# Kernel tuning notes

Measured on AMD Instinct MI355X. Metric: run time of the kernel, lower is better.

The kernel has to match this reference:

```python
import jax, jax.numpy as jnp
import numpy as np

A = -0.75  # cv2 INTER_CUBIC cubic-convolution coefficient

def _cubic_kernel(d):
    d = jnp.abs(d)
    return jnp.where(
        d <= 1.0, (A + 2.0) * d**3 - (A + 3.0) * d**2 + 1.0,
        jnp.where(d < 2.0, A * d**3 - 5.0 * A * d**2 + 8.0 * A * d - 4.0 * A, 0.0))

def _resize_last_axis(x, s):
    # Bicubic upsample along the last axis by integer factor s (half-pixel
    # aligned, replicate border), matching cv2.resize INTER_CUBIC semantics.
    n = x.shape[-1]
    out_n = n * s
    src = (jnp.arange(out_n, dtype=jnp.float32) + 0.5) / s - 0.5
    base = jnp.floor(src).astype(jnp.int32)
    t = src - base.astype(jnp.float32)
    offs = jnp.arange(-1, 3)                      # 4 taps
    w = _cubic_kernel(t[:, None] - offs[None, :].astype(jnp.float32))  # [out_n,4]
    idx = jnp.clip(base[:, None] + offs[None, :], 0, n - 1)            # [out_n,4]
    g = x[..., idx]                                # [..., out_n, 4]
    return jnp.einsum('...ok,ok->...o', g, w)

def bicubic_upscale(x, s):
    # x: [B,C,H,W] -> [B,C,H*s,W*s], separable bicubic
    y = _resize_last_axis(x, s)                    # along W
    y = jnp.swapaxes(y, -1, -2)
    y = _resize_last_axis(y, s)                    # along H
    return jnp.swapaxes(y, -1, -2)

def _conv(x, w, b, pad):
    y = jax.lax.conv_general_dilated(
        x, w, window_strides=(1, 1), padding=[(pad, pad), (pad, pad)],
        dimension_numbers=('NCHW', 'OIHW', 'NCHW'))
    return y + b[None, :, None, None]

def setup_inputs() -> dict:
    key = jax.random.key(0)
    ks = jax.random.split(key, 4)
    x = jax.random.normal(ks[0], (16, 32, 32, 4), dtype=jnp.float32)
    w1 = jax.random.normal(ks[1], (64, 4, 9, 9), dtype=jnp.float32) * (1.0 / np.sqrt(4 * 81))
    b1 = jnp.zeros((64,), jnp.float32)
    w2 = jax.random.normal(ks[2], (32, 64, 1, 1), dtype=jnp.float32) * (1.0 / np.sqrt(64))
    b2 = jnp.zeros((32,), jnp.float32)
    w3 = jax.random.normal(ks[3], (4, 32, 5, 5), dtype=jnp.float32) * (1.0 / np.sqrt(32 * 25))
    b3 = jnp.zeros((4,), jnp.float32)
    return {"x": x, "w1": w1, "b1": b1, "w2": w2, "b2": b2, "w3": w3, "b3": b3}

def reference(x, w1, b1, w2, b2, w3, b3):
    xc = jnp.transpose(x, (0, 3, 1, 2))            # NHWC -> NCHW
    up = bicubic_upscale(xc, 8)                    # [B,4,256,256]
    h = jax.nn.relu(_conv(up, w1, b1, 4))          # 9x9, 4->64
    h = jax.nn.relu(_conv(h, w2, b2, 0))           # 1x1, 64->32
    out = _conv(h, w3, b3, 2)                      # 5x5, 32->4
    return jnp.transpose(out, (0, 2, 3, 1))        # NCHW -> NHWC
```

## Files before the change

kernel.cpp:

```cpp
#include <hip/hip_runtime.h>
#include <hip/hip_bf16.h>

typedef unsigned short ushort_t;
typedef __attribute__((ext_vector_type(8))) short v8s;
typedef __attribute__((ext_vector_type(4))) float v4f;

#define B1F_F   23552
#define B2F_F   23616
#define B3F_F   23648
#define FLAG_I  23684
#define PK1_US  0
#define PK2_US  22528
#define PK3_US  26624
#define UP_US   48256
#define H2_US   4242560
#define CVT_TOTAL (47104 + 100)
#define CVT_BLOCKS 185

__device__ __forceinline__ ushort_t f2us(float v) {
  __hip_bfloat16 h = __float2bfloat16(v);
  return *reinterpret_cast<ushort_t*>(&h);
}
__device__ __forceinline__ float us2f(unsigned int u) { return __uint_as_float(u << 16); }

__device__ __forceinline__ unsigned int bfpair(float a, float b) {
  unsigned int ua = __float_as_uint(a), ub = __float_as_uint(b);
  ua += 0x7fffu + ((ua >> 16) & 1u);
  ub += 0x7fffu + ((ub >> 16) & 1u);
  return (ua >> 16) | (ub & 0xffff0000u);
}

__device__ __forceinline__ float load_in(const void* p, int i, int isbf16) {
  if (isbf16) return us2f(((const unsigned short*)p)[i]);
  return ((const float*)p)[i];
}
__device__ __forceinline__ float4 load_in4(const void* p, int i4, int isbf16) {
  if (isbf16) {
    unsigned long long q = *(const unsigned long long*)((const unsigned short*)p + i4);
    return make_float4(us2f((unsigned int)(q & 0xffff)),
                       us2f((unsigned int)((q >> 16) & 0xffff)),
                       us2f((unsigned int)((q >> 32) & 0xffff)),
                       us2f((unsigned int)((q >> 48) & 0xffff)));
  }
  return *(const float4*)((const float*)p + i4);
}

__device__ __forceinline__ float cubicw(float d) {
  const float Ac = -0.75f;
  d = fabsf(d);
  float d2 = d * d, d3 = d2 * d;
  if (d <= 1.f) return (Ac + 2.f) * d3 - (Ac + 3.f) * d2 + 1.f;
  if (d < 2.f)  return Ac * d3 - 5.f * Ac * d2 + 8.f * Ac * d - 4.f * Ac;
  return 0.f;
}

__device__ __forceinline__ int probe_dtype(const void* x) {
  __shared__ int scnt;
  const int tid = threadIdx.x;
  if (tid == 0) scnt = 0;
  __syncthreads();
  const unsigned short* xr = (const unsigned short*)x;
  int c = 0;
  for (int s = tid; s < 512; s += 256) {
    unsigned short h = xr[2 * s];
    int e = (h >> 7) & 0xFF;
    if (e >= 110 && e <= 135) c++;
  }
  if (c) atomicAdd(&scnt, c);
  __syncthreads();
  return (scnt >= 256) ? 1 : 0;
}

__global__ __launch_bounds__(256) void k_pre(
    const void* __restrict__ x,
    const void* __restrict__ w1, const void* __restrict__ b1,
    const void* __restrict__ w2, const void* __restrict__ b2,
    const void* __restrict__ w3, const void* __restrict__ b3,
    ushort_t* __restrict__ wsus, float* __restrict__ wsf,
    int* __restrict__ flag, ushort_t* __restrict__ up) {
  const int f = probe_dtype(x);
  const int tid = threadIdx.x;
  const int bid = blockIdx.x;
  if (bid == 0 && tid == 0) flag[0] = f;

  if (bid >= 4096) {
    int i = (bid - 4096) * 256 + tid;
    if (i >= CVT_TOTAL) return;
    if (i < 22528) {
      int j  = i & 7;
      int l  = (i >> 3) & 63;
      int nt = (i >> 9) & 3;
      int ks = i >> 11;
      int k  = ks * 32 + ((l >> 4) & 3) * 8 + j;
      int oc = nt * 16 + (l & 15);
      float v = 0.f;
      if (k < 324) {
        int tap = k >> 2, ic = k & 3;
        int ky = tap / 9, kx = tap - ky * 9;
        v = load_in(w1, ((oc * 4 + ic) * 9 + ky) * 9 + kx, f);
      }
      wsus[PK1_US + i] = f2us(v);
      return;
    }
    if (i < 26624) {
      int t = i - 22528;
      int j   = t & 7;
      int l   = (t >> 3) & 63;
      int mt2 = (t >> 9) & 1;
      int nt  = (t >> 10) & 3;
      int oc1 = nt * 16 + ((l >> 4) & 3) * 4 + (j & 3);
      int oc2 = mt2 * 16 + (l & 15);
      float w = load_in(w2, oc2 * 64 + oc1, f);
      float hi = us2f(f2us(w));
      wsus[PK2_US + t] = (j < 4) ? f2us(w) : f2us(w - hi);
      return;
    }
    if (i < 47104) {
      int t = i - 26624;
      int j8 = t & 7;
      int l  = (t >> 3) & 63;
      int ks = t >> 9;
      int k  = ks * 32 + ((l >> 4) & 3) * 8 + j8;
      int n  = l & 15;
      int ky = k >> 8, jj = (k >> 5) & 7, ic = k & 31;
      int dx = n >> 2, oc = n & 3;
      int kx = jj - dx;
      float w = 0.f;
      if (kx >= 0 && kx <= 4)
        w = load_in(w3, ((oc * 32 + ic) * 5 + ky) * 5 + kx, f);
      wsus[PK3_US + t] = f2us(w);
      return;
    }
    int t = i - 47104;
    if (t < 64) { wsf[B1F_F + t] = load_in(b1, t, f); return; }
    if (t < 96) { wsf[B2F_F + (t - 64)] = load_in(b2, t - 64, f); return; }
    if (t < 100) { wsf[B3F_F + (t - 96)] = load_in(b3, t - 96, f); return; }
    return;
  }

  int n = bid * 256 + tid;
  int xo = n & 255, yo = (n >> 8) & 255, b = n >> 16;
  int px = xo & 7, py = yo & 7;
  float tx = (px + 0.5f) * 0.125f + ((px >= 4) ? -0.5f : 0.5f);
  float ty = (py + 0.5f) * 0.125f + ((py >= 4) ? -0.5f : 0.5f);
  float wxa[4], wya[4];
#pragma unroll
  for (int a = 0; a < 4; a++) {
    wxa[a] = cubicw(tx - (float)(a - 1));
    wya[a] = cubicw(ty - (float)(a - 1));
  }
  int bx = (xo >> 3) + ((px >= 4) ? 0 : -1);
  int by = (yo >> 3) + ((py >= 4) ? 0 : -1);
  int ix0 = min(max(bx - 1, 0), 31), ix1 = min(max(bx, 0), 31);
  int ix2 = min(max(bx + 1, 0), 31), ix3 = min(max(bx + 2, 0), 31);
  float ax = 0.f, ay = 0.f, az = 0.f, aw = 0.f;
#pragma unroll
  for (int a = 0; a < 4; a++) {
    int iy = min(max(by + a - 1, 0), 31);
    int rowb = (b * 32 + iy) * 32;
    float4 p0 = load_in4(x, (rowb + ix0) * 4, f);
    float4 p1 = load_in4(x, (rowb + ix1) * 4, f);
    float4 p2 = load_in4(x, (rowb + ix2) * 4, f);
    float4 p3 = load_in4(x, (rowb + ix3) * 4, f);
    float rx = wxa[0] * p0.x + wxa[1] * p1.x + wxa[2] * p2.x + wxa[3] * p3.x;
    float ry = wxa[0] * p0.y + wxa[1] * p1.y + wxa[2] * p2.y + wxa[3] * p3.y;
    float rz = wxa[0] * p0.z + wxa[1] * p1.z + wxa[2] * p2.z + wxa[3] * p3.z;
    float rw = wxa[0] * p0.w + wxa[1] * p1.w + wxa[2] * p2.w + wxa[3] * p3.w;
    ax = fmaf(wya[a], rx, ax); ay = fmaf(wya[a], ry, ay);
    az = fmaf(wya[a], rz, az); aw = fmaf(wya[a], rw, aw);
  }
  unsigned long long q =
      (unsigned long long)bfpair(ax, ay) |
      ((unsigned long long)bfpair(az, aw) << 32);
  *(unsigned long long*)(up + n * 4) = q;
}

__global__ __launch_bounds__(256, 3) void k_conv12(
    const ushort_t* __restrict__ up, const ushort_t* __restrict__ wsus,
    const float* __restrict__ wsf, ushort_t* __restrict__ h2) {
  __shared__ __align__(16) ushort_t patchA[16 * 48 * 4];
  __shared__ __align__(16) ushort_t pack1L[22528];
  const int b  = blockIdx.z;
  const int x0 = blockIdx.x * 32, y0 = blockIdx.y * 8;
  const int tid = threadIdx.x;

#pragma unroll
  for (int i = 0; i < 3; ++i) {
    int e = tid + i * 256;
    int yy = e / 48, xx = e % 48;
    int gy = y0 + yy - 4, gx = x0 + xx - 4;
    unsigned long long q = 0ull;
    if (gy >= 0 && gy < 256 && gx >= 0 && gx < 256)
      q = *(const unsigned long long*)(up + (((b * 256 + gy) * 256 + gx) << 2));
    *(unsigned long long*)(patchA + e * 4) = q;
  }
  {
    const v8s* src = (const v8s*)(wsus + PK1_US);
    v8s* dst = (v8s*)pack1L;
#pragma unroll
    for (int i = 0; i < 11; ++i) {
      int e = tid + i * 256;
      dst[e] = src[e];
    }
  }

  const int lane = tid & 63, wave = tid >> 6;
  const int quad = lane >> 4, lc = lane & 15;

  int off0_v[11], off1_v[11];
#pragma unroll
  for (int ks = 0; ks < 11; ++ks) {
    int tap0 = min(ks * 8 + quad * 2, 80);
    int tap1 = min(ks * 8 + quad * 2 + 1, 80);
    int ky0 = tap0 / 9, kx0 = tap0 - ky0 * 9;
    int ky1 = tap1 / 9, kx1 = tap1 - ky1 * 9;
    off0_v[ks] = (ky0 * 48 + kx0) << 2;
    off1_v[ks] = (ky1 * 48 + kx1) << 2;
  }

  int base_m[4], pix0_[4];
#pragma unroll
  for (int i = 0; i < 4; ++i) {
    int mt = wave * 4 + i;
    int py = mt >> 1, pxh = (mt & 1) << 4;
    base_m[i] = (py * 48 + pxh + lc) << 2;
    pix0_[i] = py * 32 + pxh;
  }

  float4 b1q[4];
#pragma unroll
  for (int nt = 0; nt < 4; ++nt)
    b1q[nt] = *(const float4*)(wsf + B1F_F + nt * 16 + quad * 4);
  v4f acc[4][4];
#pragma unroll
  for (int i = 0; i < 4; ++i)
#pragma unroll
    for (int nt = 0; nt < 4; ++nt)
      acc[i][nt] = (v4f){b1q[nt].x, b1q[nt].y, b1q[nt].z, b1q[nt].w};

  __syncthreads();

  const v8s* __restrict__ Ap1 = (const v8s*)pack1L;
#pragma unroll
  for (int ks = 0; ks < 11; ++ks) {
    v8s Af[4];
#pragma unroll
    for (int nt = 0; nt < 4; ++nt) Af[nt] = Ap1[(ks * 4 + nt) * 64 + lane];
#pragma unroll
    for (int i = 0; i < 4; ++i) {
      union { unsigned long long q[2]; v8s v; } u;
      u.q[0] = *(const unsigned long long*)(patchA + base_m[i] + off0_v[ks]);
      u.q[1] = *(const unsigned long long*)(patchA + base_m[i] + off1_v[ks]);
#pragma unroll
      for (int nt = 0; nt < 4; ++nt)
        acc[i][nt] = __builtin_amdgcn_mfma_f32_16x16x32_bf16(Af[nt], u.v, acc[i][nt], 0, 0, 0);
    }
  }

  v8s w2f[4][2];
#pragma unroll
  for (int nt = 0; nt < 4; ++nt)
#pragma unroll
    for (int mt2 = 0; mt2 < 2; ++mt2)
      w2f[nt][mt2] = ((const v8s*)(wsus + PK2_US))[(nt * 2 + mt2) * 64 + lane];
  float4 b2q[2];
#pragma unroll
  for (int mt2 = 0; mt2 < 2; ++mt2)
    b2q[mt2] = *(const float4*)(wsf + B2F_F + mt2 * 16 + quad * 4);

#pragma unroll
  for (int i = 0; i < 4; ++i) {
    v4f a2[2];
#pragma unroll
    for (int mt2 = 0; mt2 < 2; ++mt2)
      a2[mt2] = (v4f){b2q[mt2].x, b2q[mt2].y, b2q[mt2].z, b2q[mt2].w};
#pragma unroll
    for (int nt = 0; nt < 4; ++nt) {
      float r0 = fmaxf(acc[i][nt][0], 0.f);
      float r1 = fmaxf(acc[i][nt][1], 0.f);
      float r2 = fmaxf(acc[i][nt][2], 0.f);
      float r3 = fmaxf(acc[i][nt][3], 0.f);
      unsigned int u0 = bfpair(r0, r1), u1 = bfpair(r2, r3);
      union { unsigned int q[4]; v8s v; } bu;
      bu.q[0] = u0; bu.q[1] = u1; bu.q[2] = u0; bu.q[3] = u1;
#pragma unroll
      for (int mt2 = 0; mt2 < 2; ++mt2)
        a2[mt2] = __builtin_amdgcn_mfma_f32_16x16x32_bf16(w2f[nt][mt2], bu.v, a2[mt2], 0, 0, 0);
    }
    int pix = pix0_[i] + lc;
    int gy = y0 + (pix >> 5), gx = x0 + (pix & 31);
    ushort_t* dst = h2 + (((b * 256 + gy) * 256 + gx) << 5) + (quad << 2);
#pragma unroll
    for (int mt2 = 0; mt2 < 2; ++mt2) {
      float v0 = fmaxf(a2[mt2][0], 0.f);
      float v1 = fmaxf(a2[mt2][1], 0.f);
      float v2 = fmaxf(a2[mt2][2], 0.f);
      float v3 = fmaxf(a2[mt2][3], 0.f);
      unsigned long long q =
          (unsigned long long)bfpair(v0, v1) |
          ((unsigned long long)bfpair(v2, v3) << 32);
      *(unsigned long long*)(dst + mt2 * 16) = q;
    }
  }
}

__global__ __launch_bounds__(256, 2) void k_conv3(
    const ushort_t* __restrict__ h2, const ushort_t* __restrict__ wsus,
    const float* __restrict__ wsf, void* __restrict__ out,
    const int* __restrict__ flag) {
  __shared__ __align__(16) ushort_t patch[20 * 1160];
  const int b  = blockIdx.z;
  const int x0 = blockIdx.x * 32, y0 = blockIdx.y * 16;
  const int tid = threadIdx.x;

  for (int e = tid; e < 720; e += 256) {
    int yy = e / 36, xx = e - yy * 36;
    int gy = y0 + yy - 2, gx = x0 + xx - 2;
    ushort_t* dst = patch + yy * 1160 + xx * 32;
    if (gy >= 0 && gy < 256 && gx >= 0 && gx < 256) {
      const ushort_t* src = h2 + (((b * 256 + gy) * 256 + gx) << 5);
#pragma unroll
      for (int c = 0; c < 4; ++c)
        *(float4*)(dst + c * 8) = *(const float4*)(src + c * 8);
    } else {
      float4 z = make_float4(0.f, 0.f, 0.f, 0.f);
#pragma unroll
      for (int c = 0; c < 4; ++c) *(float4*)(dst + c * 8) = z;
    }
  }

  const int lane = tid & 63, wave = tid >> 6;
  const int quad = lane >> 4, lc = lane & 15;

  v8s Wf[40];
  {
    const v8s* __restrict__ Bp3 = (const v8s*)(wsus + PK3_US);
#pragma unroll
    for (int ks = 0; ks < 40; ++ks) Wf[ks] = Bp3[ks * 64 + lane];
  }
  float b3v = (wsf + B3F_F)[lc & 3];
  __syncthreads();

  v4f acc[2];
  acc[0] = (v4f){b3v, b3v, b3v, b3v};
  acc[1] = (v4f){b3v, b3v, b3v, b3v};

#pragma unroll
  for (int ks = 0; ks < 40; ++ks) {
    int ky = ks >> 3, j = ks & 7;
    int rowoff = (lc + ky) * 1160 + j * 32 + quad * 8;
#pragma unroll
    for (int i = 0; i < 2; ++i) {
      int q = wave * 2 + i;
      v8s Af = *(const v8s*)(patch + rowoff + q * 128);
      acc[i] = __builtin_amdgcn_mfma_f32_16x16x32_bf16(Af, Wf[ks], acc[i], 0, 0, 0);
    }
  }

  const int fl = flag[0];
#pragma unroll
  for (int i = 0; i < 2; ++i) {
    int q = wave * 2 + i;
#pragma unroll
    for (int r = 0; r < 4; ++r) {
      int gy = y0 + (quad << 2) + r;
      int gx = x0 + (q << 2) + (lc >> 2);
      int idx = (((b * 256 + gy) * 256 + gx) << 2) + (lc & 3);
      float vv = acc[i][r];
      if (fl) ((ushort_t*)out)[idx] = f2us(vv);
      else    ((float*)out)[idx] = vv;
    }
  }
}

extern "C" void kernel_launch(void* const* d_in, const int* in_sizes, int n_in,
                              void* d_out, int out_size, void* d_ws, size_t ws_size,
                              hipStream_t stream) {
  const void* x  = d_in[0];
  const void* w1 = d_in[1];
  const void* b1 = d_in[2];
  const void* w2 = d_in[3];
  const void* b2 = d_in[4];
  const void* w3 = d_in[5];
  const void* b3 = d_in[6];

  ushort_t* wsus = (ushort_t*)d_ws;
  float* wsf = (float*)d_ws;
  int* flag = (int*)((float*)d_ws + FLAG_I);
  ushort_t* up = wsus + UP_US;
  ushort_t* h2 = wsus + H2_US;

  k_pre<<<4096 + CVT_BLOCKS, 256, 0, stream>>>(x, w1, b1, w2, b2, w3, b3,
                                               wsus, wsf, flag, up);
  k_conv12<<<dim3(8, 32, 16), 256, 0, stream>>>(up, wsus, wsf, h2);
  k_conv3<<<dim3(8, 16, 16), 256, 0, stream>>>(h2, wsus, wsf, d_out, flag);
}
```

Measured before the change: 162.4 us.

## Fuse bicubic upsample into conv1 tile loader and enlarge row tile

After: 164.9 us. No clear change (+1.5%).

```diff
diff --git a/kernel.cpp b/kernel.cpp
--- a/kernel.cpp
+++ b/kernel.cpp
@@ -12,7 +12,6 @@
 #define PK1_US  0
 #define PK2_US  22528
 #define PK3_US  26624
-#define UP_US   48256
 #define H2_US   4242560
 #define CVT_TOTAL (47104 + 100)
 #define CVT_BLOCKS 185
@@ -77,131 +76,123 @@
     const void* __restrict__ w2, const void* __restrict__ b2,
     const void* __restrict__ w3, const void* __restrict__ b3,
     ushort_t* __restrict__ wsus, float* __restrict__ wsf,
-    int* __restrict__ flag, ushort_t* __restrict__ up) {
+    int* __restrict__ flag) {
   const int f = probe_dtype(x);
   const int tid = threadIdx.x;
-  const int bid = blockIdx.x;
-  if (bid == 0 && tid == 0) flag[0] = f;
-
-  if (bid >= 4096) {
-    int i = (bid - 4096) * 256 + tid;
-    if (i >= CVT_TOTAL) return;
-    if (i < 22528) {
-      int j  = i & 7;
-      int l  = (i >> 3) & 63;
-      int nt = (i >> 9) & 3;
-      int ks = i >> 11;
-      int k  = ks * 32 + ((l >> 4) & 3) * 8 + j;
-      int oc = nt * 16 + (l & 15);
-      float v = 0.f;
-      if (k < 324) {
-        int tap = k >> 2, ic = k & 3;
-        int ky = tap / 9, kx = tap - ky * 9;
-        v = load_in(w1, ((oc * 4 + ic) * 9 + ky) * 9 + kx, f);
-      }
-      wsus[PK1_US + i] = f2us(v);
-      return;
-    }
-    if (i < 26624) {
-      int t = i - 22528;
-      int j   = t & 7;
-      int l   = (t >> 3) & 63;
-      int mt2 = (t >> 9) & 1;
-      int nt  = (t >> 10) & 3;
-      int oc1 = nt * 16 + ((l >> 4) & 3) * 4 + (j & 3);
-      int oc2 = mt2 * 16 + (l & 15);
-      float w = load_in(w2, oc2 * 64 + oc1, f);
-      float hi = us2f(f2us(w));
-      wsus[PK2_US + t] = (j < 4) ? f2us(w) : f2us(w - hi);
-      return;
-    }
-    if (i < 47104) {
-      int t = i - 26624;
-      int j8 = t & 7;
-      int l  = (t >> 3) & 63;
-      int ks = t >> 9;
-      int k  = ks * 32 + ((l >> 4) & 3) * 8 + j8;
-      int n  = l & 15;
-      int ky = k >> 8, jj = (k >> 5) & 7, ic = k & 31;
-      int dx = n >> 2, oc = n & 3;
-      int kx = jj - dx;
-      float w = 0.f;
-      if (kx >= 0 && kx <= 4)
-        w = load_in(w3, ((oc * 32 + ic) * 5 + ky) * 5 + kx, f);
-      wsus[PK3_US + t] = f2us(w);
-      return;
-    }
-    int t = i - 47104;
-    if (t < 64) { wsf[B1F_F + t] = load_in(b1, t, f); return; }
-    if (t < 96) { wsf[B2F_F + (t - 64)] = load_in(b2, t - 64, f); return; }
-    if (t < 100) { wsf[B3F_F + (t - 96)] = load_in(b3, t - 96, f); return; }
+  if (blockIdx.x == 0 && tid == 0) flag[0] = f;
+
+  int i = blockIdx.x * 256 + tid;
+  if (i >= CVT_TOTAL) return;
+  if (i < 22528) {
+    int j  = i & 7;
+    int l  = (i >> 3) & 63;
+    int nt = (i >> 9) & 3;
+    int ks = i >> 11;
+    int k  = ks * 32 + ((l >> 4) & 3) * 8 + j;
+    int oc = nt * 16 + (l & 15);
+    float v = 0.f;
+    if (k < 324) {
+      int tap = k >> 2, ic = k & 3;
+      int ky = tap / 9, kx = tap - ky * 9;
+      v = load_in(w1, ((oc * 4 + ic) * 9 + ky) * 9 + kx, f);
+    }
+    wsus[PK1_US + i] = f2us(v);
     return;
   }
-
-  int n = bid * 256 + tid;
-  int xo = n & 255, yo = (n >> 8) & 255, b = n >> 16;
-  int px = xo & 7, py = yo & 7;
-  float tx = (px + 0.5f) * 0.125f + ((px >= 4) ? -0.5f : 0.5f);
-  float ty = (py + 0.5f) * 0.125f + ((py >= 4) ? -0.5f : 0.5f);
-  float wxa[4], wya[4];
-#pragma unroll
-  for (int a = 0; a < 4; a++) {
-    wxa[a] = cubicw(tx - (float)(a - 1));
-    wya[a] = cubicw(ty - (float)(a - 1));
-  }
-  int bx = (xo >> 3) + ((px >= 4) ? 0 : -1);
-  int by = (yo >> 3) + ((py >= 4) ? 0 : -1);
-  int ix0 = min(max(bx - 1, 0), 31), ix1 = min(max(bx, 0), 31);
-  int ix2 = min(max(bx + 1, 0), 31), ix3 = min(max(bx + 2, 0), 31);
-  float ax = 0.f, ay = 0.f, az = 0.f, aw = 0.f;
-#pragma unroll
-  for (int a = 0; a < 4; a++) {
-    int iy = min(max(by + a - 1, 0), 31);
-    int rowb = (b * 32 + iy) * 32;
-    float4 p0 = load_in4(x, (rowb + ix0) * 4, f);
-    float4 p1 = load_in4(x, (rowb + ix1) * 4, f);
-    float4 p2 = load_in4(x, (rowb + ix2) * 4, f);
-    float4 p3 = load_in4(x, (rowb + ix3) * 4, f);
-    float rx = wxa[0] * p0.x + wxa[1] * p1.x + wxa[2] * p2.x + wxa[3] * p3.x;
-    float ry = wxa[0] * p0.y + wxa[1] * p1.y + wxa[2] * p2.y + wxa[3] * p3.y;
-    float rz = wxa[0] * p0.z + wxa[1] * p1.z + wxa[2] * p2.z + wxa[3] * p3.z;
-    float rw = wxa[0] * p0.w + wxa[1] * p1.w + wxa[2] * p2.w + wxa[3] * p3.w;
-    ax = fmaf(wya[a], rx, ax); ay = fmaf(wya[a], ry, ay);
-    az = fmaf(wya[a], rz, az); aw = fmaf(wya[a], rw, aw);
-  }
-  unsigned long long q =
-      (unsigned long long)bfpair(ax, ay) |
-      ((unsigned long long)bfpair(az, aw) << 32);
-  *(unsigned long long*)(up + n * 4) = q;
-}
-
-__global__ __launch_bounds__(256, 3) void k_conv12(
-    const ushort_t* __restrict__ up, const ushort_t* __restrict__ wsus,
-    const float* __restrict__ wsf, ushort_t* __restrict__ h2) {
-  __shared__ __align__(16) ushort_t patchA[16 * 48 * 4];
+  if (i < 26624) {
+    int t = i - 22528;
+    int j    = t & 7;
+    int l    = (t >> 3) & 63;
+    int mt2  = (t >> 9) & 1;
+    int p    = (t >> 10) & 1;
+    int part = (t >> 11) & 1;
+    int oc1 = (2 * p + (j >> 2)) * 16 + ((l >> 4) & 3) * 4 + (j & 3);
+    int oc2 = mt2 * 16 + (l & 15);
+    float w = load_in(w2, oc2 * 64 + oc1, f);
+    float hi = us2f(f2us(w));
+    wsus[PK2_US + t] = part ? f2us(w - hi) : f2us(w);
+    return;
+  }
+  if (i < 47104) {
+    int t = i - 26624;
+    int j8 = t & 7;
+    int l  = (t >> 3) & 63;
+    int ks = t >> 9;
+    int k  = ks * 32 + ((l >> 4) & 3) * 8 + j8;
+    int n  = l & 15;
+    int ky = k >> 8, jj = (k >> 5) & 7, ic = k & 31;
+    int dx = n >> 2, oc = n & 3;
+    int kx = jj - dx;
+    float w = 0.f;
+    if (kx >= 0 && kx <= 4)
+      w = load_in(w3, ((oc * 32 + ic) * 5 + ky) * 5 + kx, f);
+    wsus[PK3_US + t] = f2us(w);
+    return;
+  }
+  int t = i - 47104;
+  if (t < 64) { wsf[B1F_F + t] = load_in(b1, t, f); return; }
+  if (t < 96) { wsf[B2F_F + (t - 64)] = load_in(b2, t - 64, f); return; }
+  if (t < 100) { wsf[B3F_F + (t - 96)] = load_in(b3, t - 96, f); return; }
+}
+
+__global__ __launch_bounds__(256, 2) void k_conv12(
+    const void* __restrict__ x, const ushort_t* __restrict__ wsus,
+    const float* __restrict__ wsf, ushort_t* __restrict__ h2,
+    const int* __restrict__ flag) {
+  __shared__ __align__(16) ushort_t patchA[24 * 48 * 4];
   __shared__ __align__(16) ushort_t pack1L[22528];
+  __shared__ float wtab[32];
+  const int f = flag[0];
   const int b  = blockIdx.z;
-  const int x0 = blockIdx.x * 32, y0 = blockIdx.y * 8;
+  const int x0 = blockIdx.x * 32, y0 = blockIdx.y * 16;
   const int tid = threadIdx.x;
 
-#pragma unroll
-  for (int i = 0; i < 3; ++i) {
-    int e = tid + i * 256;
-    int yy = e / 48, xx = e % 48;
-    int gy = y0 + yy - 4, gx = x0 + xx - 4;
-    unsigned long long q = 0ull;
-    if (gy >= 0 && gy < 256 && gx >= 0 && gx < 256)
-      q = *(const unsigned long long*)(up + (((b * 256 + gy) * 256 + gx) << 2));
-    *(unsigned long long*)(patchA + e * 4) = q;
+  if (tid < 32) {
+    int p = tid >> 2, a = tid & 3;
+    float t = (p + 0.5f) * 0.125f + ((p >= 4) ? -0.5f : 0.5f);
+    wtab[tid] = cubicw(t - (float)(a - 1));
   }
   {
     const v8s* src = (const v8s*)(wsus + PK1_US);
     v8s* dst = (v8s*)pack1L;
 #pragma unroll
-    for (int i = 0; i < 11; ++i) {
-      int e = tid + i * 256;
-      dst[e] = src[e];
-    }
+    for (int i = 0; i < 11; ++i) dst[tid + i * 256] = src[tid + i * 256];
+  }
+  __syncthreads();
+
+  for (int e = tid; e < 1152; e += 256) {
+    int yy = e / 48, xx = e - yy * 48;
+    int gy = y0 + yy - 4, gx = x0 + xx - 4;
+    unsigned long long q = 0ull;
+    if (gy >= 0 && gy < 256 && gx >= 0 && gx < 256) {
+      int px = gx & 7, py = gy & 7;
+      float4 wx = *(const float4*)(wtab + px * 4);
+      float4 wy = *(const float4*)(wtab + py * 4);
+      int bx = (gx >> 3) + ((px >= 4) ? 0 : -1);
+      int by = (gy >> 3) + ((py >= 4) ? 0 : -1);
+      int ix0 = min(max(bx - 1, 0), 31), ix1 = min(max(bx, 0), 31);
+      int ix2 = min(max(bx + 1, 0), 31), ix3 = min(max(bx + 2, 0), 31);
+      float ax = 0.f, ay = 0.f, az = 0.f, aw = 0.f;
+      float wya[4] = {wy.x, wy.y, wy.z, wy.w};
+#pragma unroll
+      for (int a = 0; a < 4; a++) {
+        int iy = min(max(by + a - 1, 0), 31);
+        int rowb = (b * 32 + iy) * 32;
+        float4 p0 = load_in4(x, (rowb + ix0) * 4, f);
+        float4 p1 = load_in4(x, (rowb + ix1) * 4, f);
+        float4 p2 = load_in4(x, (rowb + ix2) * 4, f);
+        float4 p3 = load_in4(x, (rowb + ix3) * 4, f);
+        float rx = wx.x * p0.x + wx.y * p1.x + wx.z * p2.x + wx.w * p3.x;
+        float ry = wx.x * p0.y + wx.y * p1.y + wx.z * p2.y + wx.w * p3.y;
+        float rz = wx.x * p0.z + wx.y * p1.z + wx.z * p2.z + wx.w * p3.z;
+        float rw = wx.x * p0.w + wx.y * p1.w + wx.z * p2.w + wx.w * p3.w;
+        ax = fmaf(wya[a], rx, ax); ay = fmaf(wya[a], ry, ay);
+        az = fmaf(wya[a], rz, az); aw = fmaf(wya[a], rw, aw);
+      }
+      q = (unsigned long long)bfpair(ax, ay) |
+          ((unsigned long long)bfpair(az, aw) << 32);
+    }
+    *(unsigned long long*)(patchA + e * 4) = q;
   }
 
   const int lane = tid & 63, wave = tid >> 6;
@@ -217,23 +208,20 @@
     off0_v[ks] = (ky0 * 48 + kx0) << 2;
     off1_v[ks] = (ky1 * 48 + kx1) << 2;
   }
-
-  int base_m[4], pix0_[4];
-#pragma unroll
-  for (int i = 0; i < 4; ++i) {
-    int mt = wave * 4 + i;
-    int py = mt >> 1, pxh = (mt & 1) << 4;
+  int base_m[8];
+#pragma unroll
+  for (int i = 0; i < 8; ++i) {
+    int py = wave * 4 + (i >> 1), pxh = (i & 1) << 4;
     base_m[i] = (py * 48 + pxh + lc) << 2;
-    pix0_[i] = py * 32 + pxh;
   }
 
   float4 b1q[4];
 #pragma unroll
   for (int nt = 0; nt < 4; ++nt)
     b1q[nt] = *(const float4*)(wsf + B1F_F + nt * 16 + quad * 4);
-  v4f acc[4][4];
-#pragma unroll
-  for (int i = 0; i < 4; ++i)
+  v4f acc[8][4];
+#pragma unroll
+  for (int i = 0; i < 8; ++i)
 #pragma unroll
     for (int nt = 0; nt < 4; ++nt)
       acc[i][nt] = (v4f){b1q[nt].x, b1q[nt].y, b1q[nt].z, b1q[nt].w};
@@ -247,7 +235,7 @@
 #pragma unroll
     for (int nt = 0; nt < 4; ++nt) Af[nt] = Ap1[(ks * 4 + nt) * 64 + lane];
 #pragma unroll
-    for (int i = 0; i < 4; ++i) {
+    for (int i = 0; i < 8; ++i) {
       union { unsigned long long q[2]; v8s v; } u;
       u.q[0] = *(const unsigned long long*)(patchA + base_m[i] + off0_v[ks]);
       u.q[1] = *(const unsigned long long*)(patchA + base_m[i] + off1_v[ks]);
@@ -257,38 +245,50 @@
     }
   }
 
-  v8s w2f[4][2];
-#pragma unroll
-  for (int nt = 0; nt < 4; ++nt)
-#pragma unroll
-    for (int mt2 = 0; mt2 < 2; ++mt2)
-      w2f[nt][mt2] = ((const v8s*)(wsus + PK2_US))[(nt * 2 + mt2) * 64 + lane];
+  v8s w2f[2][2][2];
+#pragma unroll
+  for (int part = 0; part < 2; ++part)
+#pragma unroll
+    for (int p = 0; p < 2; ++p)
+#pragma unroll
+      for (int mt2 = 0; mt2 < 2; ++mt2)
+        w2f[part][p][mt2] =
+            ((const v8s*)(wsus + PK2_US))[(((part * 2 + p) * 2 + mt2)) * 64 + lane];
   float4 b2q[2];
 #pragma unroll
   for (int mt2 = 0; mt2 < 2; ++mt2)
     b2q[mt2] = *(const float4*)(wsf + B2F_F + mt2 * 16 + quad * 4);
 
 #pragma unroll
-  for (int i = 0; i < 4; ++i) {
-    v4f a2[2];
-#pragma unroll
-    for (int mt2 = 0; mt2 < 2; ++mt2)
-      a2[mt2] = (v4f){b2q[mt2].x, b2q[mt2].y, b2q[mt2].z, b2q[mt2].w};
+  for (int i = 0; i < 8; ++i) {
+    unsigned int pk[4][2];
 #pragma unroll
     for (int nt = 0; nt < 4; ++nt) {
       float r0 = fmaxf(acc[i][nt][0], 0.f);
       float r1 = fmaxf(acc[i][nt][1], 0.f);
       float r2 = fmaxf(acc[i][nt][2], 0.f);
       float r3 = fmaxf(acc[i][nt][3], 0.f);
-      unsigned int u0 = bfpair(r0, r1), u1 = bfpair(r2, r3);
+      pk[nt][0] = bfpair(r0, r1);
+      pk[nt][1] = bfpair(r2, r3);
+    }
+    v4f a2[2];
+#pragma unroll
+    for (int mt2 = 0; mt2 < 2; ++mt2)
+      a2[mt2] = (v4f){b2q[mt2].x, b2q[mt2].y, b2q[mt2].z, b2q[mt2].w};
+#pragma unroll
+    for (int p = 0; p < 2; ++p) {
       union { unsigned int q[4]; v8s v; } bu;
-      bu.q[0] = u0; bu.q[1] = u1; bu.q[2] = u0; bu.q[3] = u1;
-#pragma unroll
-      for (int mt2 = 0; mt2 < 2; ++mt2)
-        a2[mt2] = __builtin_amdgcn_mfma_f32_16x16x32_bf16(w2f[nt][mt2], bu.v, a2[mt2], 0, 0, 0);
-    }
-    int pix = pix0_[i] + lc;
-    int gy = y0 + (pix >> 5), gx = x0 + (pix & 31);
+      bu.q[0] = pk[2 * p][0]; bu.q[1] = pk[2 * p][1];
+      bu.q[2] = pk[2 * p + 1][0]; bu.q[3] = pk[2 * p + 1][1];
+#pragma unroll
+      for (int part = 0; part < 2; ++part)
+#pragma unroll
+        for (int mt2 = 0; mt2 < 2; ++mt2)
+          a2[mt2] = __builtin_amdgcn_mfma_f32_16x16x32_bf16(
+              w2f[part][p][mt2], bu.v, a2[mt2], 0, 0, 0);
+    }
+    int gy = y0 + wave * 4 + (i >> 1);
+    int gx = x0 + ((i & 1) << 4) + lc;
     ushort_t* dst = h2 + (((b * 256 + gy) * 256 + gx) << 5) + (quad << 2);
 #pragma unroll
     for (int mt2 = 0; mt2 < 2; ++mt2) {
@@ -387,11 +387,9 @@
   ushort_t* wsus = (ushort_t*)d_ws;
   float* wsf = (float*)d_ws;
   int* flag = (int*)((float*)d_ws + FLAG_I);
-  ushort_t* up = wsus + UP_US;
   ushort_t* h2 = wsus + H2_US;
 
-  k_pre<<<4096 + CVT_BLOCKS, 256, 0, stream>>>(x, w1, b1, w2, b2, w3, b3,
-                                               wsus, wsf, flag, up);
-  k_conv12<<<dim3(8, 32, 16), 256, 0, stream>>>(up, wsus, wsf, h2);
+  k_pre<<<CVT_BLOCKS, 256, 0, stream>>>(x, w1, b1, w2, b2, w3, b3, wsus, wsf, flag);
+  k_conv12<<<dim3(8, 16, 16), 256, 0, stream>>>(x, wsus, wsf, h2, flag);
   k_conv3<<<dim3(8, 16, 16), 256, 0, stream>>>(h2, wsus, wsf, d_out, flag);
 }
```
